# Optimization experiments

Hardware: AMD Instinct MI355X
Metric: run time of the kernel (lower is better)

Reference implementation:

```python
import jax, jax.numpy as jnp
import numpy as np

B, N, D, H, T, DFF, OUT = 32, 256, 512, 8, 60, 2048, 2
EPS = 1e-5


def _mha(q, k, v, Wq, Wk, Wv, Wo, bq, bk, bv, bo):
    # torch nn.MultiheadAttention (batch_first): x @ W.T + b projections
    Bq, Lq, Dm = q.shape
    dh = Dm // H
    scale = 1.0 / np.sqrt(dh).astype(np.float32)
    qh = (q @ Wq.T + bq).reshape(Bq, Lq, H, dh).transpose(0, 2, 1, 3)
    kh = (k @ Wk.T + bk).reshape(Bq, k.shape[1], H, dh).transpose(0, 2, 1, 3)
    vh = (v @ Wv.T + bv).reshape(Bq, v.shape[1], H, dh).transpose(0, 2, 1, 3)
    a = jax.nn.softmax(jnp.einsum('bhqd,bhkd->bhqk', qh, kh) * scale, axis=-1)
    o = jnp.einsum('bhqk,bhkd->bhqd', a, vh).transpose(0, 2, 1, 3).reshape(Bq, Lq, Dm)
    return o @ Wo.T + bo


def _ln(x, w, b):
    m = x.mean(-1, keepdims=True)
    v = ((x - m) ** 2).mean(-1, keepdims=True)
    return (x - m) / jnp.sqrt(v + EPS) * w + b


def setup_inputs() -> dict:
    key = jax.random.key(0)
    ks = iter(jax.random.split(key, 64))

    def rn(shape, s=0.05):
        return jax.random.normal(next(ks), shape, dtype=jnp.float32) * s

    inp = {
        'H_v_all': rn((B, N, D), 1.0),
        'H_v0_init': rn((B, 1, 1, D), 1.0),
        'pe': rn((1, T, D), 1.0),  # positional_encoding parameter
    }
    # s_* : spatial_attn;  sa_* : decoder self-attn;  ca_* : decoder cross-attn
    for p in ('s', 'sa', 'ca'):
        for m in ('Wq', 'Wk', 'Wv', 'Wo'):
            inp[f'{p}_{m}'] = rn((D, D))
        for m in ('bq', 'bk', 'bv', 'bo'):
            inp[f'{p}_{m}'] = jnp.zeros((D,), jnp.float32)
    for i in (1, 2, 3):
        inp[f'ln{i}_w'] = jnp.ones((D,), jnp.float32)
        inp[f'ln{i}_b'] = jnp.zeros((D,), jnp.float32)
    inp['W1'] = rn((DFF, D)); inp['b1'] = jnp.zeros((DFF,), jnp.float32)
    inp['W2'] = rn((D, DFF)); inp['b2'] = jnp.zeros((D,), jnp.float32)
    inp['Wout'] = rn((OUT, D)); inp['bout'] = jnp.zeros((OUT,), jnp.float32)
    return inp


def reference(H_v_all, H_v0_init, pe,
              s_Wq, s_Wk, s_Wv, s_Wo, s_bq, s_bk, s_bv, s_bo,
              sa_Wq, sa_Wk, sa_Wv, sa_Wo, sa_bq, sa_bk, sa_bv, sa_bo,
              ca_Wq, ca_Wk, ca_Wv, ca_Wo, ca_bq, ca_bk, ca_bv, ca_bo,
              ln1_w, ln1_b, ln2_w, ln2_b, ln3_w, ln3_b,
              W1, b1, W2, b2, Wout, bout):

    def dec_layer(x, mem):
        # post-norm TransformerDecoderLayer, no masks (non-causal), relu FFN, eval (no dropout)
        sa = _mha(x, x, x, sa_Wq, sa_Wk, sa_Wv, sa_Wo, sa_bq, sa_bk, sa_bv, sa_bo)
        x = _ln(x + sa, ln1_w, ln1_b)
        ca = _mha(x, mem, mem, ca_Wq, ca_Wk, ca_Wv, ca_Wo, ca_bq, ca_bk, ca_bv, ca_bo)
        x = _ln(x + ca, ln2_w, ln2_b)
        ff = jax.nn.relu(x @ W1.T + b1) @ W2.T + b2
        return _ln(x + ff, ln3_w, ln3_b)

    tgt = H_v0_init  # (B, 1, 1, D), grows along dim 2
    outputs = []
    for t in range(T):
        tgt_pe = tgt + pe[:, :t + 1][:, None]        # (B,1,t+1,D)
        tgt_step = tgt_pe.reshape(B, t + 1, D)
        ctx = _mha(tgt_step[:, -1:, :], H_v_all, H_v_all,
                   s_Wq, s_Wk, s_Wv, s_Wo, s_bq, s_bk, s_bv, s_bo)
        decoded = dec_layer(tgt_step, H_v_all)
        nxt = decoded[:, -1:, :] + ctx               # (B,1,D)
        tgt = jnp.concatenate([tgt, nxt[:, None]], axis=2)
        outputs.append(nxt[:, None])                 # (B,1,1,D)
    out_seq = jnp.concatenate(outputs, axis=2)       # (B,1,T,D)
    return out_seq @ Wout.T + bout                   # (B,1,T,2)
```

## Files before the change

### kernel.cpp

```cpp
#include <hip/hip_runtime.h>


#define NB 32
#define NN 256
#define DD 512
#define NH 8
#define DH 64
#define TT 60
#define DF 2048
#define NBLK 256
#define NTHR 512

typedef unsigned short ushort_t;
typedef _Float16 half2v __attribute__((ext_vector_type(2)));

constexpr size_t SZ_KV  = (size_t)NB * NN * DD;
constexpr size_t SZ_ROW = (size_t)NB * DD;
constexpr size_t SZ_PAR = (size_t)NB * NH * DD;
constexpr size_t SZ_SAB = (size_t)NB * NH * TT * DH;
constexpr size_t OFF_KS32 = 0;
constexpr size_t OFF_VS32 = SZ_KV;
constexpr size_t OFF_KC32 = 2 * SZ_KV;
constexpr size_t OFF_VC32 = 3 * SZ_KV;
constexpr size_t OFF_X    = 0;
constexpr size_t OFF_U1P  = OFF_X   + SZ_ROW;
constexpr size_t OFF_U2P  = OFF_U1P + SZ_PAR;
constexpr size_t OFF_U3P  = OFF_U2P + SZ_PAR;
constexpr size_t OFF_CTP0 = OFF_U3P + SZ_PAR;
constexpr size_t OFF_CTP1 = OFF_CTP0 + SZ_PAR;
constexpr size_t OFF_BF   = 4 * SZ_KV;
constexpr size_t UOFF_KST = 0;
constexpr size_t UOFF_KCT = SZ_KV;
constexpr size_t UOFF_VSH = 2 * SZ_KV;
constexpr size_t UOFF_VCH = 3 * SZ_KV;
constexpr size_t UOFF_KSA = 4 * SZ_KV;
constexpr size_t UOFF_VSA = UOFF_KSA + SZ_SAB;
constexpr size_t UOFF_W8  = UOFF_VSA + SZ_SAB;
constexpr size_t UOFF_W1  = UOFF_W8 + 8ull * DD * DD;
constexpr size_t UOFF_W2  = UOFF_W1 + (size_t)DD * DF;
constexpr size_t UEND     = UOFF_W2 + (size_t)DF * DD;
constexpr size_t OFF_FLG  = OFF_BF + (UEND + 1) / 2;

constexpr unsigned DYN_LDS = 131072;

__device__ __forceinline__ float ldg_a(const float* p) {
  return __hip_atomic_load(p, __ATOMIC_RELAXED, __HIP_MEMORY_SCOPE_AGENT);
}
__device__ __forceinline__ void stg_a(float* p, float v) {
  __hip_atomic_store(p, v, __ATOMIC_RELAXED, __HIP_MEMORY_SCOPE_AGENT);
}
__device__ __forceinline__ unsigned f2pk(float a, float b) {
  return __builtin_bit_cast(unsigned, __builtin_amdgcn_cvt_pkrtz(a, b));
}
__device__ __forceinline__ ushort_t f2h(float a) {
  return (ushort_t)(f2pk(a, 0.f) & 0xffffu);
}
__device__ __forceinline__ float h2f(ushort_t u) {
  return (float)__builtin_bit_cast(_Float16, u);
}
__device__ __forceinline__ float fdot2u(unsigned a, unsigned b, float c) {
  return __builtin_amdgcn_fdot2(__builtin_bit_cast(half2v, a),
                                __builtin_bit_cast(half2v, b), c, false);
}

struct Params {
  const float *pe;
  const float *sa_bq, *sa_bk, *sa_bv, *s_bq, *sa_bo, *s_bo, *ca_bq, *ca_bo;
  const float *ln1w, *ln1b, *ln2w, *ln2b, *ln3w, *ln3b;
  const float *b1, *b2, *Wout, *bout;
  const ushort_t *w8, *w1b, *w2b;
  const ushort_t *KsT, *KcT, *VsH, *VcH;
  ushort_t *KsaB, *VsaB;
  float *xcur, *u1p, *u2p, *u3p, *ctp0, *ctp1;
  float *out;
  unsigned *flags;
};

__device__ __forceinline__ void gbar(unsigned* fl, int tid, int h,
                                     unsigned& rnd) {
  __builtin_amdgcn_s_waitcnt(0);
  __syncthreads();
  rnd++;
  if (tid < 64) {
    if (tid == h)
      __hip_atomic_store(&fl[h], rnd, __ATOMIC_RELAXED,
                         __HIP_MEMORY_SCOPE_AGENT);
    bool wait = true;
    while (wait) {
      unsigned v = rnd;
      if (tid < 8)
        v = __hip_atomic_load(&fl[tid], __ATOMIC_RELAXED,
                              __HIP_MEMORY_SCOPE_AGENT);
      wait = __any(v < rnd);
    }
  }
  __syncthreads();
}

__global__ __launch_bounds__(512) void decode_persistent(Params P) {
  __shared__ __align__(16) float sX[2048];
  __shared__ __align__(16) float sPart[512];
  __shared__ float sAux[64];
  __shared__ __align__(16) float xrow[512];
  __shared__ __align__(16) float y1s[512];
  __shared__ __align__(16) float zs[512];
  __shared__ __align__(16) unsigned xh[256];
  __shared__ __align__(16) unsigned ph[512];
  extern __shared__ __align__(16) unsigned dynLds[];
  unsigned* Ks_l = dynLds;
  unsigned* Kc_l = dynLds + 8192;
  ushort_t* Vs_l = (ushort_t*)(dynLds + 16384);
  ushort_t* Vc_l = Vs_l + 16384;

  int tid = threadIdx.x;
  int bid = blockIdx.x;
  int b = bid >> 3, h = bid & 7;
  int idx8 = bid;
  unsigned* fl = P.flags + b * 64;
  unsigned rnd = 0;

  {
    const uint4* gks = (const uint4*)((const unsigned*)P.KsT +
                       (((size_t)b * DD + h * DH) >> 1) * NN);
    const uint4* gkc = (const uint4*)((const unsigned*)P.KcT +
                       (((size_t)b * DD + h * DH) >> 1) * NN);
    const uint4* gvs = (const uint4*)(P.VsH + (size_t)idx8 * NN * DH);
    const uint4* gvc = (const uint4*)(P.VcH + (size_t)idx8 * NN * DH);
    uint4* dks = (uint4*)Ks_l;
    uint4* dkc = (uint4*)Kc_l;
    uint4* dvs = (uint4*)Vs_l;
    uint4* dvc = (uint4*)Vc_l;
    #pragma unroll
    for (int i = 0; i < 4; i++) {
      int idx = i * NTHR + tid;
      dks[idx] = gks[idx];
      dkc[idx] = gkc[idx];
      dvs[idx] = gvs[idx];
      dvc[idx] = gvc[idx];
    }
  }

  xrow[tid] = ldg_a(P.xcur + (size_t)b * DD + tid);
  __syncthreads();
  if (tid < 256) xh[tid] = f2pk(xrow[2 * tid], xrow[2 * tid + 1]);
  __syncthreads();

  for (int t = 0; t < TT; t++) {
    {
      {
        int w = tid >> 6, c = tid & 63, m = w >> 1, half = w & 1;
        int col = h * DH + c;
        const uint2* wp = (const uint2*)(P.w8 + (size_t)m * DD * DD) + col;
        float acc = 0.f;
        #pragma unroll 8
        for (int kq = half * 64; kq < half * 64 + 64; kq++) {
          uint2 wv = wp[(size_t)kq * DD];
          uint2 xv = *(const uint2*)&xh[kq * 2];
          acc = fdot2u(wv.x, xv.x, acc);
          acc = fdot2u(wv.y, xv.y, acc);
        }
        sPart[tid] = acc;
      }
      __syncthreads();
      if (tid < 256) {
        int m = tid >> 6, c = tid & 63, col = h * DH + c;
        const float* bias = (m == 0) ? P.sa_bq : (m == 1) ? P.sa_bk
                          : (m == 2) ? P.sa_bv : P.s_bq;
        float val = sPart[(2 * m) * 64 + c] + sPart[(2 * m + 1) * 64 + c]
                    + bias[col];
        sX[512 + tid] = val;
        if (m == 1) P.KsaB[((size_t)idx8 * TT + t) * DH + c] = f2h(val);
        if (m == 2) P.VsaB[((size_t)idx8 * TT + t) * DH + c] = f2h(val);
      }
      __syncthreads();

      int L = t + 1;
      float* sQ  = sX + 512;
      float* sQs = sX + 704;
      float* sPb = sX + 768;
      float* sB  = sX + 1024;
      if (tid < 64) {
        float sc = -1e30f;
        if (tid < L) {
          const ushort_t* kp = P.KsaB + ((size_t)idx8 * TT + tid) * DH;
          float a = 0.f;
          #pragma unroll
          for (int i = 0; i < DH; i += 4) {
            ushort4 kv = *(const ushort4*)(kp + i);
            a += sQ[i] * h2f(kv.x) + sQ[i + 1] * h2f(kv.y) +
                 sQ[i + 2] * h2f(kv.z) + sQ[i + 3] * h2f(kv.w);
          }
          sc = a * 0.125f;
        }
        float mx = sc;
        #pragma unroll
        for (int s = 32; s >= 1; s >>= 1) mx = fmaxf(mx, __shfl_xor(mx, s));
        float e = (tid < L) ? __expf(sc - mx) : 0.f;
        float s2 = e;
        #pragma unroll
        for (int s = 32; s >= 1; s >>= 1) s2 += __shfl_xor(s2, s);
        sPb[tid] = e;
        if (tid == 0) sAux[12] = 1.f / s2;
      } else if (tid < 96) {
        int i = tid - 64;
        ph[i] = f2pk(sQs[2 * i], sQs[2 * i + 1]);
      }
      __syncthreads();
      {
        int g = tid >> 6, d = tid & 63;
        float a2 = 0.f;
        for (int j = g; j < L; j += 8)
          a2 += sPb[j] * h2f(P.VsaB[((size_t)idx8 * TT + j) * DH + d]);
        sB[tid] = a2;
      }
      __syncthreads();
      if (tid < 64) {
        float o = 0.f;
        #pragma unroll
        for (int i = 0; i < 8; i++) o += sB[i * 64 + tid];
        sX[tid] = o * sAux[12];
      }
      __syncthreads();

      {
        int n = tid & 255, dh2 = tid >> 8;
        const unsigned* kp = Ks_l + n;
        float a = 0.f;
        #pragma unroll 8
        for (int dw = dh2 * 16; dw < dh2 * 16 + 16; dw++)
          a = fdot2u(kp[dw * NN], ph[dw], a);
        sPart[tid] = a;
      }
      __syncthreads();
      float* sPr = sX + 1536;
      if (tid < 256) {
        float sc = (sPart[tid] + sPart[256 + tid]) * 0.125f;
        sPr[tid] = sc;
        int w = tid >> 6, lane = tid & 63;
        float mx = sc;
        #pragma unroll
        for (int s = 32; s >= 1; s >>= 1) mx = fmaxf(mx, __shfl_xor(mx, s));
        if (lane == 0) sAux[w] = mx;
      }
      __syncthreads();
      if (tid < 256) {
        int w = tid >> 6, lane = tid & 63;
        float mx = fmaxf(fmaxf(sAux[0], sAux[1]), fmaxf(sAux[2], sAux[3]));
        float e = __expf(sPr[tid] - mx);
        sPr[tid] = e;
        float s2 = e;
        #pragma unroll
        for (int s = 32; s >= 1; s >>= 1) s2 += __shfl_xor(s2, s);
        if (lane == 0) sAux[4 + w] = s2;
      }
      __syncthreads();
      {
        int g = tid >> 6, d = tid & 63;
        float inv = 1.f / (sAux[4] + sAux[5] + sAux[6] + sAux[7]);
        const ushort_t* vp = Vs_l + (g * 32) * DH + d;
        float acc = 0.f;
        #pragma unroll 4
        for (int n = 0; n < 32; n++) acc += sPr[g * 32 + n] * h2f(vp[n * DH]);
        sB[tid] = acc * inv;
      }
      __syncthreads();
      if (tid < 64) {
        float o = 0.f;
        #pragma unroll
        for (int i = 0; i < 8; i++) o += sB[i * 64 + tid];
        sX[64 + tid] = o;
      }
      __syncthreads();
      if (tid < 64)
        ph[32 + tid] = f2pk(sX[2 * tid], sX[2 * tid + 1]);
      __syncthreads();

      {
        float* ctp = ((t & 1) ? P.ctp1 : P.ctp0) + ((size_t)b * NH + h) * DD;
        float* u1p = P.u1p + ((size_t)b * NH + h) * DD;
        const uint2* wpa = (const uint2*)(P.w8 + 4ull * DD * DD) + tid;
        const uint2* wpb = (const uint2*)(P.w8 + 5ull * DD * DD) + tid;
        float acc1 = (h == 0) ? P.sa_bo[tid] + xrow[tid] : 0.f;
        float acc2 = (h == 0) ? P.s_bo[tid] : 0.f;
        #pragma unroll 8
        for (int j = 0; j < 16; j++) {
          int k4 = h * 16 + j;
          uint2 wv = wpa[(size_t)k4 * DD];
          uint2 x1 = *(const uint2*)&ph[32 + 2 * j];
          acc1 = fdot2u(wv.x, x1.x, acc1);
          acc1 = fdot2u(wv.y, x1.y, acc1);
          uint2 wv2 = wpb[(size_t)k4 * DD];
          uint2 x2 = *(const uint2*)&ph[64 + 2 * j];
          acc2 = fdot2u(wv2.x, x2.x, acc2);
          acc2 = fdot2u(wv2.y, x2.y, acc2);
        }
        stg_a(&u1p[tid], acc1);
        stg_a(&ctp[tid], acc2);
      }
    }
    gbar(fl, tid, h, rnd);

    {
      float u = 0.f;
      {
        const float* pp = P.u1p + (size_t)b * NH * DD + tid;
        #pragma unroll
        for (int i = 0; i < 8; i++) u += ldg_a(pp + i * DD);
      }
      {
        int w = tid >> 6, lane = tid & 63;
        float s = u, q2 = u * u;
        #pragma unroll
        for (int m = 32; m >= 1; m >>= 1) { s += __shfl_xor(s, m); q2 += __shfl_xor(q2, m); }
        if (lane == 0) { sAux[w] = s; sAux[8 + w] = q2; }
      }
      __syncthreads();
      {
        float ss = 0.f, qq = 0.f;
        #pragma unroll
        for (int i = 0; i < 8; i++) { ss += sAux[i]; qq += sAux[8 + i]; }
        float mean = ss * (1.f / 512.f);
        float inv = rsqrtf(qq * (1.f / 512.f) - mean * mean + 1e-5f);
        y1s[tid] = (u - mean) * inv * P.ln1w[tid] + P.ln1b[tid];
      }
      __syncthreads();
      if (tid < 256) ph[128 + tid] = f2pk(y1s[2 * tid], y1s[2 * tid + 1]);
      __syncthreads();
      {
        int c = tid & 63, w = tid >> 6, col = h * DH + c;
        const uint2* wp = (const uint2*)(P.w8 + 6ull * DD * DD) + col;
        float acc = 0.f;
        #pragma unroll 8
        for (int kq = w * 16; kq < w * 16 + 16; kq++) {
          uint2 wv = wp[(size_t)kq * DD];
          uint2 xv = *(const uint2*)&ph[128 + 2 * kq];
          acc = fdot2u(wv.x, xv.x, acc);
          acc = fdot2u(wv.y, xv.y, acc);
        }
        sPart[tid] = acc;
      }
      __syncthreads();
      float* sQc = sX + 512;
      if (tid < 64) {
        float acc = 0.f;
        #pragma unroll
        for (int i = 0; i < 8; i++) acc += sPart[i * 64 + tid];
        sQc[tid] = acc + P.ca_bq[h * DH + tid];
      }
      __syncthreads();
      if (tid < 32) ph[tid] = f2pk(sQc[2 * tid], sQc[2 * tid + 1]);
      __syncthreads();
      {
        int n = tid & 255, dh2 = tid >> 8;
        const unsigned* kp = Kc_l + n;
        float a = 0.f;
        #pragma unroll 8
        for (int dw = dh2 * 16; dw < dh2 * 16 + 16; dw++)
          a = fdot2u(kp[dw * NN], ph[dw], a);
        sPart[tid] = a;
      }
      __syncthreads();
      float* sPr = sX + 1536;
      if (tid < 256) {
        float sc = (sPart[tid] + sPart[256 + tid]) * 0.125f;
        sPr[tid] = sc;
        int w = tid >> 6, lane = tid & 63;
        float mx = sc;
        #pragma unroll
        for (int s = 32; s >= 1; s >>= 1) mx = fmaxf(mx, __shfl_xor(mx, s));
        if (lane == 0) sAux[w] = mx;
      }
      __syncthreads();
      if (tid < 256) {
        int w = tid >> 6, lane = tid & 63;
        float mx = fmaxf(fmaxf(sAux[0], sAux[1]), fmaxf(sAux[2], sAux[3]));
        float e = __expf(sPr[tid] - mx);
        sPr[tid] = e;
        float s2 = e;
        #pragma unroll
        for (int s = 32; s >= 1; s >>= 1) s2 += __shfl_xor(s2, s);
        if (lane == 0) sAux[4 + w] = s2;
      }
      __syncthreads();
      float* sB = sX + 1024;
      {
        int g = tid >> 6, d = tid & 63;
        float inv = 1.f / (sAux[4] + sAux[5] + sAux[6] + sAux[7]);
        const ushort_t* vp = Vc_l + (g * 32) * DH + d;
        float acc = 0.f;
        #pragma unroll 4
        for (int n = 0; n < 32; n++) acc += sPr[g * 32 + n] * h2f(vp[n * DH]);
        sB[tid] = acc * inv;
      }
      __syncthreads();
      if (tid < 64) {
        float o = 0.f;
        #pragma unroll
        for (int i = 0; i < 8; i++) o += sB[i * 64 + tid];
        sX[tid] = o;
      }
      __syncthreads();
      if (tid < 32) ph[32 + tid] = f2pk(sX[2 * tid], sX[2 * tid + 1]);
      __syncthreads();
      {
        const uint2* wp = (const uint2*)(P.w8 + 7ull * DD * DD) + tid;
        float acc = (h == 0) ? P.ca_bo[tid] + y1s[tid] : 0.f;
        #pragma unroll 8
        for (int j = 0; j < 16; j++) {
          int k4 = h * 16 + j;
          uint2 wv = wp[(size_t)k4 * DD];
          uint2 xv = *(const uint2*)&ph[32 + 2 * j];
          acc = fdot2u(wv.x, xv.x, acc);
          acc = fdot2u(wv.y, xv.y, acc);
        }
        stg_a(&P.u2p[((size_t)b * NH + h) * DD + tid], acc);
      }
    }
    gbar(fl, tid, h, rnd);

    {
      float v = 0.f;
      {
        const float* pp = P.u2p + (size_t)b * NH * DD + tid;
        #pragma unroll
        for (int i = 0; i < 8; i++) v += ldg_a(pp + i * DD);
      }
      {
        int w = tid >> 6, lane = tid & 63;
        float s = v, q2 = v * v;
        #pragma unroll
        for (int m = 32; m >= 1; m >>= 1) { s += __shfl_xor(s, m); q2 += __shfl_xor(q2, m); }
        if (lane == 0) { sAux[w] = s; sAux[8 + w] = q2; }
      }
      __syncthreads();
      {
        float ss = 0.f, qq = 0.f;
        #pragma unroll
        for (int i = 0; i < 8; i++) { ss += sAux[i]; qq += sAux[8 + i]; }
        float mean = ss * (1.f / 512.f);
        float inv = rsqrtf(qq * (1.f / 512.f) - mean * mean + 1e-5f);
        zs[tid] = (v - mean) * inv * P.ln2w[tid] + P.ln2b[tid];
      }
      __syncthreads();
      if (tid < 256) ph[128 + tid] = f2pk(zs[2 * tid], zs[2 * tid + 1]);
      __syncthreads();
      {
        int c = tid & 255, half = tid >> 8, col = h * 256 + c;
        const uint2* wp = (const uint2*)P.w1b + col;
        float acc = 0.f;
        #pragma unroll 8
        for (int kq = half * 64; kq < half * 64 + 64; kq++) {
          uint2 wv = wp[(size_t)kq * DF];
          uint2 xv = *(const uint2*)&ph[128 + 2 * kq];
          acc = fdot2u(wv.x, xv.x, acc);
          acc = fdot2u(wv.y, xv.y, acc);
        }
        sPart[tid] = acc;
      }
      __syncthreads();
      float* hh = sX;
      if (tid < 256)
        hh[tid] = fmaxf(sPart[tid] + sPart[256 + tid] + P.b1[h * 256 + tid], 0.f);
      __syncthreads();
      if (tid < 128) ph[384 + tid] = f2pk(hh[2 * tid], hh[2 * tid + 1]);
      __syncthreads();
      {
        const uint2* wp = (const uint2*)P.w2b + tid;
        float acc = (h == 0) ? zs[tid] + P.b2[tid] : 0.f;
        #pragma unroll 8
        for (int j = 0; j < 64; j++) {
          int k4 = h * 64 + j;
          uint2 wv = wp[(size_t)k4 * DD];
          uint2 xv = *(const uint2*)&ph[384 + 2 * j];
          acc = fdot2u(wv.x, xv.x, acc);
          acc = fdot2u(wv.y, xv.y, acc);
        }
        stg_a(&P.u3p[((size_t)b * NH + h) * DD + tid], acc);
      }
    }
    gbar(fl, tid, h, rnd);

    {
      float u = 0.f, ctxv = 0.f;
      {
        const float* pp = P.u3p + (size_t)b * NH * DD + tid;
        const float* cp = ((t & 1) ? P.ctp1 : P.ctp0) + (size_t)b * NH * DD + tid;
        #pragma unroll
        for (int i = 0; i < 8; i++) { u += ldg_a(pp + i * DD); ctxv += ldg_a(cp + i * DD); }
      }
      {
        int w = tid >> 6, lane = tid & 63;
        float s = u, q2 = u * u;
        #pragma unroll
        for (int m = 32; m >= 1; m >>= 1) { s += __shfl_xor(s, m); q2 += __shfl_xor(q2, m); }
        if (lane == 0) { sAux[w] = s; sAux[8 + w] = q2; }
      }
      __syncthreads();
      float ss = 0.f, qq = 0.f;
      #pragma unroll
      for (int i = 0; i < 8; i++) { ss += sAux[i]; qq += sAux[8 + i]; }
      float mean = ss * (1.f / 512.f);
      float inv = rsqrtf(qq * (1.f / 512.f) - mean * mean + 1e-5f);
      float nxt = (u - mean) * inv * P.ln3w[tid] + P.ln3b[tid] + ctxv;
      float p = (t < TT - 1) ? P.pe[(size_t)(t + 1) * DD + tid] : 0.f;
      if (h == 0) sX[tid] = nxt;
      __syncthreads();
      xrow[tid] = nxt + p;
      if (h == 0) {
        {
          int c = tid >> 8, l = tid & 255;
          float a = sX[l] * P.Wout[(size_t)c * DD + l] +
                    sX[l + 256] * P.Wout[(size_t)c * DD + l + 256];
          #pragma unroll
          for (int m = 32; m >= 1; m >>= 1) a += __shfl_xor(a, m);
          if ((tid & 63) == 0) sAux[16 + (tid >> 6)] = a;
        }
        __syncthreads();
        if (tid == 0)
          P.out[((size_t)b * TT + t) * 2 + 0] =
              sAux[16] + sAux[17] + sAux[18] + sAux[19] + P.bout[0];
        if (tid == 256)
          P.out[((size_t)b * TT + t) * 2 + 1] =
              sAux[20] + sAux[21] + sAux[22] + sAux[23] + P.bout[1];
      }
      __syncthreads();
      if (tid < 256) xh[tid] = f2pk(xrow[2 * tid], xrow[2 * tid + 1]);
      __syncthreads();
    }
  }
}

__global__ __launch_bounds__(256) void gemm_kv(
    const float* __restrict__ A,
    const float* __restrict__ W0, const float* __restrict__ W1_,
    const float* __restrict__ W2_, const float* __restrict__ W3_,
    const float* __restrict__ b0, const float* __restrict__ b1_,
    const float* __restrict__ b2_, const float* __restrict__ b3_,
    float* __restrict__ O0, float* __restrict__ O1,
    float* __restrict__ O2, float* __restrict__ O3) {
  __shared__ __align__(16) float As[8][128];
  __shared__ __align__(16) float Bs[8][128];
  int tid = threadIdx.x;
  int bx = blockIdx.x, by = blockIdx.y;
  int mm = bx >> 2;
  int col0 = (bx & 3) * 128;
  const float* W = mm == 0 ? W0 : mm == 1 ? W1_ : mm == 2 ? W2_ : W3_;
  const float* bias = mm == 0 ? b0 : mm == 1 ? b1_ : mm == 2 ? b2_ : b3_;
  float* O = mm == 0 ? O0 : mm == 1 ? O1 : mm == 2 ? O2 : O3;
  int tx = tid & 15, ty = tid >> 4;
  int m0 = by * 128;
  int lr = tid >> 1, lk = (tid & 1) * 4;
  const float* Ap = A + (size_t)(m0 + lr) * DD + lk;
  const float* Wp = W + (size_t)(col0 + lr) * DD + lk;
  float c[8][8] = {};
  for (int k0 = 0; k0 < DD; k0 += 8) {
    float4 av = *(const float4*)(Ap + k0);
    float4 wv = *(const float4*)(Wp + k0);
    __syncthreads();
    As[lk + 0][lr] = av.x; As[lk + 1][lr] = av.y; As[lk + 2][lr] = av.z; As[lk + 3][lr] = av.w;
    Bs[lk + 0][lr] = wv.x; Bs[lk + 1][lr] = wv.y; Bs[lk + 2][lr] = wv.z; Bs[lk + 3][lr] = wv.w;
    __syncthreads();
    #pragma unroll
    for (int k = 0; k < 8; k++) {
      float a[8], bb[8];
      *(float4*)&a[0] = *(const float4*)&As[k][ty * 8];
      *(float4*)&a[4] = *(const float4*)&As[k][ty * 8 + 4];
      *(float4*)&bb[0] = *(const float4*)&Bs[k][tx * 8];
      *(float4*)&bb[4] = *(const float4*)&Bs[k][tx * 8 + 4];
      #pragma unroll
      for (int i = 0; i < 8; i++)
        #pragma unroll
        for (int j = 0; j < 8; j++) c[i][j] += a[i] * bb[j];
    }
  }
  const float* bp = bias + col0 + tx * 8;
  for (int i = 0; i < 8; i++) {
    int row = m0 + ty * 8 + i;
    float* op = O + (size_t)row * DD + col0 + tx * 8;
    #pragma unroll
    for (int jq = 0; jq < 8; jq += 4) {
      float4 v;
      v.x = c[i][jq + 0] + bp[jq + 0];
      v.y = c[i][jq + 1] + bp[jq + 1];
      v.z = c[i][jq + 2] + bp[jq + 2];
      v.w = c[i][jq + 3] + bp[jq + 3];
      *(float4*)(op + jq) = v;
    }
  }
}

__global__ __launch_bounds__(256) void pack_kT(const float* __restrict__ Ks32,
                                               const float* __restrict__ Kc32,
                                               ushort_t* __restrict__ KsT,
                                               ushort_t* __restrict__ KcT) {
  int z = blockIdx.z;
  int b = z >> 1;
  const float* in = ((z & 1) ? Kc32 : Ks32) + (size_t)b * NN * DD;
  ushort_t* out = ((z & 1) ? KcT : KsT) + (size_t)b * NN * DD;
  int r0 = blockIdx.x * 32, c0 = blockIdx.y * 32;
  __shared__ float tile[32][33];
  int tid = threadIdx.x;
  int i = tid >> 3, j4 = (tid & 7) * 4;
  float4 v = *(const float4*)(in + (size_t)(r0 + i) * DD + c0 + j4);
  tile[i][j4] = v.x; tile[i][j4 + 1] = v.y; tile[i][j4 + 2] = v.z; tile[i][j4 + 3] = v.w;
  __syncthreads();
  int d = c0 + i;
  ushort_t* op = out + (size_t)(d >> 1) * (2 * NN) + 2 * (r0 + j4) + (d & 1);
  op[0] = f2h(tile[j4][i]);     op[2] = f2h(tile[j4 + 1][i]);
  op[4] = f2h(tile[j4 + 2][i]); op[6] = f2h(tile[j4 + 3][i]);
}

__global__ __launch_bounds__(256) void pack_vh(const float* __restrict__ Vs32,
                                               const float* __restrict__ Vc32,
                                               ushort_t* __restrict__ VsH,
                                               ushort_t* __restrict__ VcH) {
  const float* src = blockIdx.y ? Vc32 : Vs32;
  ushort_t* dst = blockIdx.y ? VcH : VsH;
  size_t idx = (size_t)blockIdx.x * 1024 + threadIdx.x * 4;
  float4 v = *(const float4*)(src + idx);
  int d512 = (int)(idx & 511);
  int n = (int)((idx >> 9) & 255);
  int b = (int)(idx >> 17);
  int h = d512 >> 6, d = d512 & 63;
  ushort_t* op = dst + (((size_t)(b * 8 + h) * NN + n) * DH + d);
  op[0] = f2h(v.x); op[1] = f2h(v.y); op[2] = f2h(v.z); op[3] = f2h(v.w);
}

struct PWItem { const float* in; ushort_t* out; int C; int K; };
struct PWArgs { PWItem m[10]; };
__global__ __launch_bounds__(256) void pack_w(PWArgs a) {
  PWItem it = a.m[blockIdx.y];
  int total = it.C * (it.K >> 2);
  int e = blockIdx.x * 256 + threadIdx.x;
  if (e >= total) return;
  int kd = it.K >> 2;
  int k4 = e % kd, col = e / kd;
  float4 v = *(const float4*)(it.in + (size_t)col * it.K + k4 * 4);
  unsigned lo = f2pk(v.x, v.y), hi = f2pk(v.z, v.w);
  ushort4 o;
  o.x = (ushort_t)(lo & 0xffffu); o.y = (ushort_t)(lo >> 16);
  o.z = (ushort_t)(hi & 0xffffu); o.w = (ushort_t)(hi >> 16);
  *((ushort4*)it.out + (size_t)k4 * it.C + col) = o;
}

__global__ __launch_bounds__(256) void init_x(const float* __restrict__ hv0,
                                              const float* __restrict__ pe,
                                              float* __restrict__ ws,
                                              unsigned* __restrict__ flags) {
  int i = blockIdx.x * 256 + threadIdx.x;
  ws[OFF_X + i] = hv0[i] + pe[i & (DD - 1)];
  if (i < 2048) flags[i] = 0u;
}

extern "C" void kernel_launch(void* const* d_in, const int* in_sizes, int n_in,
                              void* d_out, int out_size, void* d_ws, size_t ws_size,
                              hipStream_t stream) {
  const float* H_v_all = (const float*)d_in[0];
  const float* H_v0    = (const float*)d_in[1];
  const float* pe      = (const float*)d_in[2];
  const float* s_Wq = (const float*)d_in[3];
  const float* s_Wk = (const float*)d_in[4];
  const float* s_Wv = (const float*)d_in[5];
  const float* s_Wo = (const float*)d_in[6];
  const float* s_bq = (const float*)d_in[7];
  const float* s_bk = (const float*)d_in[8];
  const float* s_bv = (const float*)d_in[9];
  const float* s_bo = (const float*)d_in[10];
  const float* sa_Wq = (const float*)d_in[11];
  const float* sa_Wk = (const float*)d_in[12];
  const float* sa_Wv = (const float*)d_in[13];
  const float* sa_Wo = (const float*)d_in[14];
  const float* sa_bq = (const float*)d_in[15];
  const float* sa_bk = (const float*)d_in[16];
  const float* sa_bv = (const float*)d_in[17];
  const float* sa_bo = (const float*)d_in[18];
  const float* ca_Wq = (const float*)d_in[19];
  const float* ca_Wk = (const float*)d_in[20];
  const float* ca_Wv = (const float*)d_in[21];
  const float* ca_Wo = (const float*)d_in[22];
  const float* ca_bq = (const float*)d_in[23];
  const float* ca_bk = (const float*)d_in[24];
  const float* ca_bv = (const float*)d_in[25];
  const float* ca_bo = (const float*)d_in[26];
  const float* ln1w = (const float*)d_in[27];
  const float* ln1b = (const float*)d_in[28];
  const float* ln2w = (const float*)d_in[29];
  const float* ln2b = (const float*)d_in[30];
  const float* ln3w = (const float*)d_in[31];
  const float* ln3b = (const float*)d_in[32];
  const float* W1   = (const float*)d_in[33];
  const float* b1   = (const float*)d_in[34];
  const float* W2   = (const float*)d_in[35];
  const float* b2   = (const float*)d_in[36];
  const float* Wout = (const float*)d_in[37];
  const float* bout = (const float*)d_in[38];

  float* ws = (float*)d_ws;
  float* Ks32 = ws + OFF_KS32;
  float* Vs32 = ws + OFF_VS32;
  float* Kc32 = ws + OFF_KC32;
  float* Vc32 = ws + OFF_VC32;
  ushort_t* ub = (ushort_t*)(ws + OFF_BF);
  unsigned* flags = (unsigned*)(ws + OFF_FLG);

  hipLaunchKernelGGL(gemm_kv, dim3(16, 64), dim3(256), 0, stream,
                     H_v_all, s_Wk, s_Wv, ca_Wk, ca_Wv,
                     s_bk, s_bv, ca_bk, ca_bv, Ks32, Vs32, Kc32, Vc32);

  hipLaunchKernelGGL(pack_kT, dim3(8, 16, 64), dim3(256), 0, stream,
                     Ks32, Kc32, ub + UOFF_KST, ub + UOFF_KCT);
  hipLaunchKernelGGL(pack_vh, dim3((unsigned)(SZ_KV / 1024), 2), dim3(256), 0,
                     stream, Vs32, Vc32, ub + UOFF_VSH, ub + UOFF_VCH);

  PWArgs pw;
  pw.m[0] = {sa_Wq, ub + UOFF_W8 + 0ull * DD * DD, DD, DD};
  pw.m[1] = {sa_Wk, ub + UOFF_W8 + 1ull * DD * DD, DD, DD};
  pw.m[2] = {sa_Wv, ub + UOFF_W8 + 2ull * DD * DD, DD, DD};
  pw.m[3] = {s_Wq,  ub + UOFF_W8 + 3ull * DD * DD, DD, DD};
  pw.m[4] = {sa_Wo, ub + UOFF_W8 + 4ull * DD * DD, DD, DD};
  pw.m[5] = {s_Wo,  ub + UOFF_W8 + 5ull * DD * DD, DD, DD};
  pw.m[6] = {ca_Wq, ub + UOFF_W8 + 6ull * DD * DD, DD, DD};
  pw.m[7] = {ca_Wo, ub + UOFF_W8 + 7ull * DD * DD, DD, DD};
  pw.m[8] = {W1, ub + UOFF_W1, DF, DD};
  pw.m[9] = {W2, ub + UOFF_W2, DD, DF};
  hipLaunchKernelGGL(pack_w, dim3(1024, 10), dim3(256), 0, stream, pw);

  hipLaunchKernelGGL(init_x, dim3(64), dim3(256), 0, stream,
                     H_v0, pe, ws, flags);

  static bool attr_set = false;
  if (!attr_set) {
    hipFuncSetAttribute((const void*)decode_persistent,
                        hipFuncAttributeMaxDynamicSharedMemorySize, DYN_LDS);
    attr_set = true;
  }

  Params P;
  P.pe = pe;
  P.sa_bq = sa_bq; P.sa_bk = sa_bk; P.sa_bv = sa_bv; P.s_bq = s_bq;
  P.sa_bo = sa_bo; P.s_bo = s_bo; P.ca_bq = ca_bq; P.ca_bo = ca_bo;
  P.ln1w = ln1w; P.ln1b = ln1b; P.ln2w = ln2w; P.ln2b = ln2b;
  P.ln3w = ln3w; P.ln3b = ln3b;
  P.b1 = b1; P.b2 = b2; P.Wout = Wout; P.bout = bout;
  P.w8 = ub + UOFF_W8; P.w1b = ub + UOFF_W1; P.w2b = ub + UOFF_W2;
  P.KsT = ub + UOFF_KST; P.KcT = ub + UOFF_KCT;
  P.VsH = ub + UOFF_VSH; P.VcH = ub + UOFF_VCH;
  P.KsaB = ub + UOFF_KSA; P.VsaB = ub + UOFF_VSA;
  P.xcur = ws + OFF_X;
  P.u1p = ws + OFF_U1P; P.u2p = ws + OFF_U2P; P.u3p = ws + OFF_U3P;
  P.ctp0 = ws + OFF_CTP0; P.ctp1 = ws + OFF_CTP1;
  P.out = (float*)d_out;
  P.flags = flags;

  void* kargs[] = { (void*)&P };
  hipLaunchCooperativeKernel((void*)decode_persistent, dim3(NBLK), dim3(NTHR),
                             kargs, DYN_LDS, stream);
}
```

Measured before the change: 2.208 ms.

## Keep self-attn KV cache in LDS, prefetch weights, drop softmax max and barriers

Moves the per-block self-attention K/V cache from global memory into shared memory, and prefetches the output-projection and cross-attn weights into registers before the attention phases. It merges self-attention scoring, softmax and value accumulation into one wave, and runs that wave concurrently with the spatial-attention scoring. Softmax max-subtraction is removed, and several LDS staging buffers and __syncthreads are replaced by shuffle-based fp16 packing. The cost is many extra registers under a (512,2) launch bound, plus a risk of exp overflow for large attention scores.

Result: slower. 5.877 ms (+166.1%).

```diff
diff --git a/kernel.cpp b/kernel.cpp
--- a/kernel.cpp
+++ b/kernel.cpp
@@ -70,7 +70,6 @@
   const float *b1, *b2, *Wout, *bout;
   const ushort_t *w8, *w1b, *w2b;
   const ushort_t *KsT, *KcT, *VsH, *VcH;
-  ushort_t *KsaB, *VsaB;
   float *xcur, *u1p, *u2p, *u3p, *ctp0, *ctp1;
   float *out;
   unsigned *flags;
@@ -97,15 +96,14 @@
   __syncthreads();
 }
 
-__global__ __launch_bounds__(512) void decode_persistent(Params P) {
+__global__ __launch_bounds__(512, 2) void decode_persistent(Params P) {
   __shared__ __align__(16) float sX[2048];
   __shared__ __align__(16) float sPart[512];
   __shared__ float sAux[64];
-  __shared__ __align__(16) float xrow[512];
-  __shared__ __align__(16) float y1s[512];
-  __shared__ __align__(16) float zs[512];
   __shared__ __align__(16) unsigned xh[256];
-  __shared__ __align__(16) unsigned ph[512];
+  __shared__ __align__(16) unsigned ph[384];
+  __shared__ __align__(16) ushort_t cacheK[TT * 78];
+  __shared__ __align__(16) ushort_t cacheV[TT * 64];
   extern __shared__ __align__(16) unsigned dynLds[];
   unsigned* Ks_l = dynLds;
   unsigned* Kc_l = dynLds + 8192;
@@ -140,9 +138,11 @@
     }
   }
 
-  xrow[tid] = ldg_a(P.xcur + (size_t)b * DD + tid);
-  __syncthreads();
-  if (tid < 256) xh[tid] = f2pk(xrow[2 * tid], xrow[2 * tid + 1]);
+  float x_f = ldg_a(P.xcur + (size_t)b * DD + tid);
+  {
+    float px = __shfl_xor(x_f, 1);
+    if (!(tid & 1)) xh[tid >> 1] = f2pk(x_f, px);
+  }
   __syncthreads();
 
   for (int t = 0; t < TT; t++) {
@@ -169,91 +169,71 @@
         float val = sPart[(2 * m) * 64 + c] + sPart[(2 * m + 1) * 64 + c]
                     + bias[col];
         sX[512 + tid] = val;
-        if (m == 1) P.KsaB[((size_t)idx8 * TT + t) * DH + c] = f2h(val);
-        if (m == 2) P.VsaB[((size_t)idx8 * TT + t) * DH + c] = f2h(val);
-      }
-      __syncthreads();
-
+        if (m == 1) cacheK[t * 78 + c] = f2h(val);
+        if (m == 2) cacheV[t * 64 + c] = f2h(val);
+      }
+      __syncthreads();
+
+      uint2 wA[16], wB[16];
+      {
+        const uint2* wpa = (const uint2*)(P.w8 + 4ull * DD * DD) + tid;
+        const uint2* wpb = (const uint2*)(P.w8 + 5ull * DD * DD) + tid;
+        #pragma unroll
+        for (int j = 0; j < 16; j++) {
+          wA[j] = wpa[(size_t)(h * 16 + j) * DD];
+          wB[j] = wpb[(size_t)(h * 16 + j) * DD];
+        }
+      }
       int L = t + 1;
       float* sQ  = sX + 512;
       float* sQs = sX + 704;
       float* sPb = sX + 768;
-      float* sB  = sX + 1024;
       if (tid < 64) {
-        float sc = -1e30f;
+        float e = 0.f;
         if (tid < L) {
-          const ushort_t* kp = P.KsaB + ((size_t)idx8 * TT + tid) * DH;
+          const unsigned* kl = (const unsigned*)(cacheK + (size_t)tid * 78);
           float a = 0.f;
-          #pragma unroll
-          for (int i = 0; i < DH; i += 4) {
-            ushort4 kv = *(const ushort4*)(kp + i);
-            a += sQ[i] * h2f(kv.x) + sQ[i + 1] * h2f(kv.y) +
-                 sQ[i + 2] * h2f(kv.z) + sQ[i + 3] * h2f(kv.w);
+          #pragma unroll 8
+          for (int i = 0; i < 32; i++) {
+            unsigned w = kl[i];
+            a += sQ[2 * i] * h2f((ushort_t)(w & 0xffffu)) +
+                 sQ[2 * i + 1] * h2f((ushort_t)(w >> 16));
           }
-          sc = a * 0.125f;
-        }
-        float mx = sc;
-        #pragma unroll
-        for (int s = 32; s >= 1; s >>= 1) mx = fmaxf(mx, __shfl_xor(mx, s));
-        float e = (tid < L) ? __expf(sc - mx) : 0.f;
+          e = __expf(a * 0.125f);
+        }
         float s2 = e;
         #pragma unroll
         for (int s = 32; s >= 1; s >>= 1) s2 += __shfl_xor(s2, s);
-        sPb[tid] = e;
-        if (tid == 0) sAux[12] = 1.f / s2;
-      } else if (tid < 96) {
-        int i = tid - 64;
-        ph[i] = f2pk(sQs[2 * i], sQs[2 * i + 1]);
-      }
-      __syncthreads();
-      {
-        int g = tid >> 6, d = tid & 63;
-        float a2 = 0.f;
-        for (int j = g; j < L; j += 8)
-          a2 += sPb[j] * h2f(P.VsaB[((size_t)idx8 * TT + j) * DH + d]);
-        sB[tid] = a2;
-      }
-      __syncthreads();
-      if (tid < 64) {
+        sPb[tid] = e * (1.f / s2);
         float o = 0.f;
-        #pragma unroll
-        for (int i = 0; i < 8; i++) o += sB[i * 64 + tid];
-        sX[tid] = o * sAux[12];
-      }
-      __syncthreads();
-
-      {
-        int n = tid & 255, dh2 = tid >> 8;
-        const unsigned* kp = Ks_l + n;
+        for (int j = 0; j < L; j++)
+          o += sPb[j] * h2f(cacheV[j * 64 + tid]);
+        float po = __shfl_xor(o, 1);
+        if (!(tid & 1)) ph[32 + (tid >> 1)] = f2pk(o, po);
+      } else if (tid < 320) {
+        int n = tid - 64;
         float a = 0.f;
         #pragma unroll 8
-        for (int dw = dh2 * 16; dw < dh2 * 16 + 16; dw++)
-          a = fdot2u(kp[dw * NN], ph[dw], a);
-        sPart[tid] = a;
+        for (int i = 0; i < 32; i++) {
+          unsigned w = Ks_l[i * NN + n];
+          a += sQs[2 * i] * h2f((ushort_t)(w & 0xffffu)) +
+               sQs[2 * i + 1] * h2f((ushort_t)(w >> 16));
+        }
+        sPart[n] = a * 0.125f;
       }
       __syncthreads();
       float* sPr = sX + 1536;
       if (tid < 256) {
-        float sc = (sPart[tid] + sPart[256 + tid]) * 0.125f;
-        sPr[tid] = sc;
-        int w = tid >> 6, lane = tid & 63;
-        float mx = sc;
-        #pragma unroll
-        for (int s = 32; s >= 1; s >>= 1) mx = fmaxf(mx, __shfl_xor(mx, s));
-        if (lane == 0) sAux[w] = mx;
-      }
-      __syncthreads();
-      if (tid < 256) {
-        int w = tid >> 6, lane = tid & 63;
-        float mx = fmaxf(fmaxf(sAux[0], sAux[1]), fmaxf(sAux[2], sAux[3]));
-        float e = __expf(sPr[tid] - mx);
+        float e = __expf(sPart[tid]);
         sPr[tid] = e;
+        int w = tid >> 6;
         float s2 = e;
         #pragma unroll
         for (int s = 32; s >= 1; s >>= 1) s2 += __shfl_xor(s2, s);
-        if (lane == 0) sAux[4 + w] = s2;
-      }
-      __syncthreads();
+        if ((tid & 63) == 0) sAux[4 + w] = s2;
+      }
+      __syncthreads();
+      float* sB = sX + 1024;
       {
         int g = tid >> 6, d = tid & 63;
         float inv = 1.f / (sAux[4] + sAux[5] + sAux[6] + sAux[7]);
@@ -268,31 +248,23 @@
         float o = 0.f;
         #pragma unroll
         for (int i = 0; i < 8; i++) o += sB[i * 64 + tid];
-        sX[64 + tid] = o;
-      }
-      __syncthreads();
-      if (tid < 64)
-        ph[32 + tid] = f2pk(sX[2 * tid], sX[2 * tid + 1]);
-      __syncthreads();
-
+        float po = __shfl_xor(o, 1);
+        if (!(tid & 1)) ph[64 + (tid >> 1)] = f2pk(o, po);
+      }
+      __syncthreads();
       {
         float* ctp = ((t & 1) ? P.ctp1 : P.ctp0) + ((size_t)b * NH + h) * DD;
         float* u1p = P.u1p + ((size_t)b * NH + h) * DD;
-        const uint2* wpa = (const uint2*)(P.w8 + 4ull * DD * DD) + tid;
-        const uint2* wpb = (const uint2*)(P.w8 + 5ull * DD * DD) + tid;
-        float acc1 = (h == 0) ? P.sa_bo[tid] + xrow[tid] : 0.f;
+        float acc1 = (h == 0) ? P.sa_bo[tid] + x_f : 0.f;
         float acc2 = (h == 0) ? P.s_bo[tid] : 0.f;
         #pragma unroll 8
         for (int j = 0; j < 16; j++) {
-          int k4 = h * 16 + j;
-          uint2 wv = wpa[(size_t)k4 * DD];
           uint2 x1 = *(const uint2*)&ph[32 + 2 * j];
-          acc1 = fdot2u(wv.x, x1.x, acc1);
-          acc1 = fdot2u(wv.y, x1.y, acc1);
-          uint2 wv2 = wpb[(size_t)k4 * DD];
+          acc1 = fdot2u(wA[j].x, x1.x, acc1);
+          acc1 = fdot2u(wA[j].y, x1.y, acc1);
           uint2 x2 = *(const uint2*)&ph[64 + 2 * j];
-          acc2 = fdot2u(wv2.x, x2.x, acc2);
-          acc2 = fdot2u(wv2.y, x2.y, acc2);
+          acc2 = fdot2u(wB[j].x, x2.x, acc2);
+          acc2 = fdot2u(wB[j].y, x2.y, acc2);
         }
         stg_a(&u1p[tid], acc1);
         stg_a(&ctp[tid], acc2);
@@ -300,6 +272,7 @@
     }
     gbar(fl, tid, h, rnd);
 
+    float y1f;
     {
       float u = 0.f;
       {
@@ -307,12 +280,23 @@
         #pragma unroll
         for (int i = 0; i < 8; i++) u += ldg_a(pp + i * DD);
       }
-      {
-        int w = tid >> 6, lane = tid & 63;
+      uint2 wq[16], wu[16];
+      {
+        int c = tid & 63, w = tid >> 6;
+        const uint2* wpq = (const uint2*)(P.w8 + 6ull * DD * DD) + (h * DH + c);
+        const uint2* wpu = (const uint2*)(P.w8 + 7ull * DD * DD) + tid;
+        #pragma unroll
+        for (int j = 0; j < 16; j++) {
+          wq[j] = wpq[(size_t)(w * 16 + j) * DD];
+          wu[j] = wpu[(size_t)(h * 16 + j) * DD];
+        }
+      }
+      {
+        int w = tid >> 6;
         float s = u, q2 = u * u;
         #pragma unroll
         for (int m = 32; m >= 1; m >>= 1) { s += __shfl_xor(s, m); q2 += __shfl_xor(q2, m); }
-        if (lane == 0) { sAux[w] = s; sAux[8 + w] = q2; }
+        if ((tid & 63) == 0) { sAux[w] = s; sAux[8 + w] = q2; }
       }
       __syncthreads();
       {
@@ -321,65 +305,51 @@
         for (int i = 0; i < 8; i++) { ss += sAux[i]; qq += sAux[8 + i]; }
         float mean = ss * (1.f / 512.f);
         float inv = rsqrtf(qq * (1.f / 512.f) - mean * mean + 1e-5f);
-        y1s[tid] = (u - mean) * inv * P.ln1w[tid] + P.ln1b[tid];
-      }
-      __syncthreads();
-      if (tid < 256) ph[128 + tid] = f2pk(y1s[2 * tid], y1s[2 * tid + 1]);
-      __syncthreads();
-      {
-        int c = tid & 63, w = tid >> 6, col = h * DH + c;
-        const uint2* wp = (const uint2*)(P.w8 + 6ull * DD * DD) + col;
+        y1f = (u - mean) * inv * P.ln1w[tid] + P.ln1b[tid];
+        float py = __shfl_xor(y1f, 1);
+        if (!(tid & 1)) ph[128 + (tid >> 1)] = f2pk(y1f, py);
+      }
+      __syncthreads();
+      {
+        int w = tid >> 6;
         float acc = 0.f;
         #pragma unroll 8
-        for (int kq = w * 16; kq < w * 16 + 16; kq++) {
-          uint2 wv = wp[(size_t)kq * DD];
+        for (int j = 0; j < 16; j++) {
+          int kq = w * 16 + j;
           uint2 xv = *(const uint2*)&ph[128 + 2 * kq];
-          acc = fdot2u(wv.x, xv.x, acc);
-          acc = fdot2u(wv.y, xv.y, acc);
+          acc = fdot2u(wq[j].x, xv.x, acc);
+          acc = fdot2u(wq[j].y, xv.y, acc);
         }
         sPart[tid] = acc;
       }
       __syncthreads();
-      float* sQc = sX + 512;
       if (tid < 64) {
-        float acc = 0.f;
-        #pragma unroll
-        for (int i = 0; i < 8; i++) acc += sPart[i * 64 + tid];
-        sQc[tid] = acc + P.ca_bq[h * DH + tid];
-      }
-      __syncthreads();
-      if (tid < 32) ph[tid] = f2pk(sQc[2 * tid], sQc[2 * tid + 1]);
+        float o = 0.f;
+        #pragma unroll
+        for (int i = 0; i < 8; i++) o += sPart[i * 64 + tid];
+        o += P.ca_bq[h * DH + tid];
+        float po = __shfl_xor(o, 1);
+        if (!(tid & 1)) ph[tid >> 1] = f2pk(o, po);
+      }
       __syncthreads();
       {
         int n = tid & 255, dh2 = tid >> 8;
-        const unsigned* kp = Kc_l + n;
         float a = 0.f;
         #pragma unroll 8
         for (int dw = dh2 * 16; dw < dh2 * 16 + 16; dw++)
-          a = fdot2u(kp[dw * NN], ph[dw], a);
+          a = fdot2u(Kc_l[dw * NN + n], ph[dw], a);
         sPart[tid] = a;
       }
       __syncthreads();
       float* sPr = sX + 1536;
       if (tid < 256) {
-        float sc = (sPart[tid] + sPart[256 + tid]) * 0.125f;
-        sPr[tid] = sc;
-        int w = tid >> 6, lane = tid & 63;
-        float mx = sc;
-        #pragma unroll
-        for (int s = 32; s >= 1; s >>= 1) mx = fmaxf(mx, __shfl_xor(mx, s));
-        if (lane == 0) sAux[w] = mx;
-      }
-      __syncthreads();
-      if (tid < 256) {
-        int w = tid >> 6, lane = tid & 63;
-        float mx = fmaxf(fmaxf(sAux[0], sAux[1]), fmaxf(sAux[2], sAux[3]));
-        float e = __expf(sPr[tid] - mx);
+        float e = __expf((sPart[tid] + sPart[256 + tid]) * 0.125f);
         sPr[tid] = e;
+        int w = tid >> 6;
         float s2 = e;
         #pragma unroll
         for (int s = 32; s >= 1; s >>= 1) s2 += __shfl_xor(s2, s);
-        if (lane == 0) sAux[4 + w] = s2;
+        if ((tid & 63) == 0) sAux[4 + w] = s2;
       }
       __syncthreads();
       float* sB = sX + 1024;
@@ -397,27 +367,24 @@
         float o = 0.f;
         #pragma unroll
         for (int i = 0; i < 8; i++) o += sB[i * 64 + tid];
-        sX[tid] = o;
-      }
-      __syncthreads();
-      if (tid < 32) ph[32 + tid] = f2pk(sX[2 * tid], sX[2 * tid + 1]);
-      __syncthreads();
-      {
-        const uint2* wp = (const uint2*)(P.w8 + 7ull * DD * DD) + tid;
-        float acc = (h == 0) ? P.ca_bo[tid] + y1s[tid] : 0.f;
+        float po = __shfl_xor(o, 1);
+        if (!(tid & 1)) ph[32 + (tid >> 1)] = f2pk(o, po);
+      }
+      __syncthreads();
+      {
+        float acc = (h == 0) ? P.ca_bo[tid] + y1f : 0.f;
         #pragma unroll 8
         for (int j = 0; j < 16; j++) {
-          int k4 = h * 16 + j;
-          uint2 wv = wp[(size_t)k4 * DD];
           uint2 xv = *(const uint2*)&ph[32 + 2 * j];
-          acc = fdot2u(wv.x, xv.x, acc);
-          acc = fdot2u(wv.y, xv.y, acc);
+          acc = fdot2u(wu[j].x, xv.x, acc);
+          acc = fdot2u(wu[j].y, xv.y, acc);
         }
         stg_a(&P.u2p[((size_t)b * NH + h) * DD + tid], acc);
       }
     }
     gbar(fl, tid, h, rnd);
 
+    float zf;
     {
       float v = 0.f;
       {
@@ -426,11 +393,11 @@
         for (int i = 0; i < 8; i++) v += ldg_a(pp + i * DD);
       }
       {
-        int w = tid >> 6, lane = tid & 63;
+        int w = tid >> 6;
         float s = v, q2 = v * v;
         #pragma unroll
         for (int m = 32; m >= 1; m >>= 1) { s += __shfl_xor(s, m); q2 += __shfl_xor(q2, m); }
-        if (lane == 0) { sAux[w] = s; sAux[8 + w] = q2; }
+        if ((tid & 63) == 0) { sAux[w] = s; sAux[8 + w] = q2; }
       }
       __syncthreads();
       {
@@ -439,10 +406,10 @@
         for (int i = 0; i < 8; i++) { ss += sAux[i]; qq += sAux[8 + i]; }
         float mean = ss * (1.f / 512.f);
         float inv = rsqrtf(qq * (1.f / 512.f) - mean * mean + 1e-5f);
-        zs[tid] = (v - mean) * inv * P.ln2w[tid] + P.ln2b[tid];
-      }
-      __syncthreads();
-      if (tid < 256) ph[128 + tid] = f2pk(zs[2 * tid], zs[2 * tid + 1]);
+        zf = (v - mean) * inv * P.ln2w[tid] + P.ln2b[tid];
+        float pz = __shfl_xor(zf, 1);
+        if (!(tid & 1)) ph[128 + (tid >> 1)] = f2pk(zf, pz);
+      }
       __syncthreads();
       {
         int c = tid & 255, half = tid >> 8, col = h * 256 + c;
@@ -458,20 +425,20 @@
         sPart[tid] = acc;
       }
       __syncthreads();
-      float* hh = sX;
-      if (tid < 256)
-        hh[tid] = fmaxf(sPart[tid] + sPart[256 + tid] + P.b1[h * 256 + tid], 0.f);
-      __syncthreads();
-      if (tid < 128) ph[384 + tid] = f2pk(hh[2 * tid], hh[2 * tid + 1]);
+      if (tid < 256) {
+        float hv = fmaxf(sPart[tid] + sPart[256 + tid] + P.b1[h * 256 + tid], 0.f);
+        float pv = __shfl_xor(hv, 1);
+        if (!(tid & 1)) ph[tid >> 1] = f2pk(hv, pv);
+      }
       __syncthreads();
       {
         const uint2* wp = (const uint2*)P.w2b + tid;
-        float acc = (h == 0) ? zs[tid] + P.b2[tid] : 0.f;
+        float acc = (h == 0) ? zf + P.b2[tid] : 0.f;
         #pragma unroll 8
         for (int j = 0; j < 64; j++) {
           int k4 = h * 64 + j;
           uint2 wv = wp[(size_t)k4 * DD];
-          uint2 xv = *(const uint2*)&ph[384 + 2 * j];
+          uint2 xv = *(const uint2*)&ph[2 * j];
           acc = fdot2u(wv.x, xv.x, acc);
           acc = fdot2u(wv.y, xv.y, acc);
         }
@@ -489,11 +456,11 @@
         for (int i = 0; i < 8; i++) { u += ldg_a(pp + i * DD); ctxv += ldg_a(cp + i * DD); }
       }
       {
-        int w = tid >> 6, lane = tid & 63;
+        int w = tid >> 6;
         float s = u, q2 = u * u;
         #pragma unroll
         for (int m = 32; m >= 1; m >>= 1) { s += __shfl_xor(s, m); q2 += __shfl_xor(q2, m); }
-        if (lane == 0) { sAux[w] = s; sAux[8 + w] = q2; }
+        if ((tid & 63) == 0) { sAux[w] = s; sAux[8 + w] = q2; }
       }
       __syncthreads();
       float ss = 0.f, qq = 0.f;
@@ -503,9 +470,13 @@
       float inv = rsqrtf(qq * (1.f / 512.f) - mean * mean + 1e-5f);
       float nxt = (u - mean) * inv * P.ln3w[tid] + P.ln3b[tid] + ctxv;
       float p = (t < TT - 1) ? P.pe[(size_t)(t + 1) * DD + tid] : 0.f;
+      x_f = nxt + p;
+      {
+        float px = __shfl_xor(x_f, 1);
+        if (!(tid & 1)) xh[tid >> 1] = f2pk(x_f, px);
+      }
       if (h == 0) sX[tid] = nxt;
       __syncthreads();
-      xrow[tid] = nxt + p;
       if (h == 0) {
         {
           int c = tid >> 8, l = tid & 255;
@@ -523,8 +494,6 @@
           P.out[((size_t)b * TT + t) * 2 + 1] =
               sAux[20] + sAux[21] + sAux[22] + sAux[23] + P.bout[1];
       }
-      __syncthreads();
-      if (tid < 256) xh[tid] = f2pk(xrow[2 * tid], xrow[2 * tid + 1]);
       __syncthreads();
     }
   }
@@ -745,7 +714,6 @@
   P.w8 = ub + UOFF_W8; P.w1b = ub + UOFF_W1; P.w2b = ub + UOFF_W2;
   P.KsT = ub + UOFF_KST; P.KcT = ub + UOFF_KCT;
   P.VsH = ub + UOFF_VSH; P.VcH = ub + UOFF_VCH;
-  P.KsaB = ub + UOFF_KSA; P.VsaB = ub + UOFF_VSA;
   P.xcur = ws + OFF_X;
   P.u1p = ws + OFF_U1P; P.u2p = ws + OFF_U2P; P.u3p = ws + OFF_U3P;
   P.ctp0 = ws + OFF_CTP0; P.ctp1 = ws + OFF_CTP1;
```
